# Kernel tuning notes

Hardware: AMD Instinct MI355X
Metric: run time of the kernel (lower is better)

The kernel has to match this reference:

```python
import jax, jax.numpy as jnp
import numpy as np
from jax import lax

# --- constants matching init_kwargs ---
NUM_SCALES = 3
LAMBDA_0, MU_0 = 1.0, 0.5
KAPPA_LAMBDA, KAPPA_MU = 2.0, 1.0
BASE_WEIGHT, GRADIENT_SCALING = 1.0, 5.0
CLAMP_MIN, CLAMP_MAX = 0.1, 10.0
SCALE_WEIGHTS = [1.0, 0.5, 0.25]
JAC_PENALTY_W = 0.1
BLUR_KSIZE, BLUR_SIGMA = 5, 1.1  # torchvision default sigma for ksize=5: 0.3*((5-1)*0.5-1)+0.8


def _resize1d_align_corners(x, axis, out_size):
    """Linear resize along one axis with align_corners=True (separable trilinear)."""
    n = x.shape[axis]
    if out_size == n:
        return x
    coords = jnp.arange(out_size, dtype=jnp.float32) * ((n - 1) / max(out_size - 1, 1))
    i0 = jnp.floor(coords).astype(jnp.int32)
    i1 = jnp.minimum(i0 + 1, n - 1)
    w = (coords - i0.astype(jnp.float32)).astype(x.dtype)
    shape = [1] * x.ndim
    shape[axis] = out_size
    w = w.reshape(shape)
    x0 = jnp.take(x, i0, axis=axis)
    x1 = jnp.take(x, i1, axis=axis)
    return x0 * (1 - w) + x1 * w


def trilinear_resize(x, out_sizes):
    # x: (B, C, X, Y, Z); align_corners=True trilinear is separable
    for ax, s in zip((-3, -2, -1), out_sizes):
        x = _resize1d_align_corners(x, ax % x.ndim, s)
    return x


def _blur_axis(x, axis, k):
    r = (BLUR_KSIZE - 1) // 2
    pad = [(0, 0)] * x.ndim
    pad[axis] = (r, r)
    xp = jnp.pad(x, pad, mode='reflect')
    n = x.shape[axis]
    out = jnp.zeros_like(x)
    for t in range(BLUR_KSIZE):
        out = out + k[t] * lax.slice_in_dim(xp, t, t + n, axis=axis)
    return out


def gaussian_blur3d(x):
    t = jnp.arange(BLUR_KSIZE, dtype=jnp.float32) - (BLUR_KSIZE - 1) / 2
    k = jnp.exp(-(t ** 2) / (2.0 * BLUR_SIGMA ** 2))
    k = (k / k.sum()).astype(x.dtype)
    for ax in (-3, -2, -1):
        x = _blur_axis(x, ax % x.ndim, k)
    return x


def jacobian_penalty(deform):
    # 3x3 Jacobian of the displacement at the center voxel via central differences
    B, _, X, Y, Z = deform.shape
    c = (X // 2, Y // 2, Z // 2)
    dx = 0.5 * (deform[:, :, c[0] + 1, c[1], c[2]] - deform[:, :, c[0] - 1, c[1], c[2]])
    dy = 0.5 * (deform[:, :, c[0], c[1] + 1, c[2]] - deform[:, :, c[0], c[1] - 1, c[2]])
    dz = 0.5 * (deform[:, :, c[0], c[1], c[2] + 1] - deform[:, :, c[0], c[1], c[2] - 1])
    J = jnp.stack([dx, dy, dz], axis=-1)  # (B, 3, 3)
    det = jnp.linalg.det(J)
    return jnp.mean(jax.nn.relu(-det))


def _loss_fwd(deformation_field, image):
    B, _, X, Y, Z = deformation_field.shape
    total = jnp.zeros((), dtype=deformation_field.dtype)
    for i in range(NUM_SCALES):
        scale = 2 ** i
        out_sizes = (X // scale, Y // scale, Z // scale)
        deform_s = trilinear_resize(deformation_field, out_sizes)
        image_s = trilinear_resize(image, out_sizes)
        img = image_s[:, 0]  # (B, x, y, z)
        gx, gy, gz = jnp.gradient(img, axis=(-3, -2, -1))
        image_gradient = jnp.sqrt(gx ** 2 + gy ** 2 + gz ** 2)
        ig_sm = gaussian_blur3d(image_gradient[None])  # (1, B, x, y, z)
        lam = jnp.clip(LAMBDA_0 + KAPPA_LAMBDA * ig_sm, CLAMP_MIN, CLAMP_MAX)
        mu = jnp.clip(MU_0 + KAPPA_MU * ig_sm, CLAMP_MIN, CLAMP_MAX)
        du = jnp.gradient(deform_s[:, 0], axis=(-3, -2, -1))
        dv = jnp.gradient(deform_s[:, 1], axis=(-3, -2, -1))
        dw = jnp.gradient(deform_s[:, 2], axis=(-3, -2, -1))
        E_xx, E_yy, E_zz = du[0], dv[1], dw[2]
        E_xy = 0.5 * (du[1] + dv[0])
        E_xz = 0.5 * (du[2] + dw[0])
        E_yz = 0.5 * (dv[2] + dw[1])
        trace_E = E_xx + E_yy + E_zz
        energy = (0.5 * lam * trace_E ** 2
                  + mu * (E_xx ** 2 + E_yy ** 2 + E_zz ** 2
                          + 2.0 * (E_xy ** 2 + E_xz ** 2 + E_yz ** 2)))
        weight = BASE_WEIGHT + GRADIENT_SCALING * ig_sm
        total = total + SCALE_WEIGHTS[i] * jnp.mean(weight * energy)
    total = total + JAC_PENALTY_W * jacobian_penalty(deformation_field)
    return total


def setup_inputs() -> dict:
    key = jax.random.key(0)
    k1, k2 = jax.random.split(key)
    deformation_field = jax.random.normal(k1, (2, 3, 160, 160, 160), dtype=jnp.float32)
    image = jax.random.uniform(k2, (2, 1, 160, 160, 160), dtype=jnp.float32)
    return {"deformation_field": deformation_field, "image": image}


def reference(deformation_field, image):
    return _loss_fwd(deformation_field, image)
```

## Files before the change

### kernel.cpp

```cpp
#include <hip/hip_runtime.h>

#define TPB 256

#define K0 0.0707663f
#define K1 0.2444606f
#define K2 0.3695462f

#define EB0 8000
#define EB1 1000
#define EB2 125
#define BB0 2000
#define BB1 250
#define BB2 32

typedef float f4 __attribute__((ext_vector_type(4)));

__device__ __forceinline__ f4 ld4(const float* __restrict__ p) { return *(const f4*)p; }

__device__ __forceinline__ int rref(int i, int n) {
    return i < 0 ? -i : (i >= n ? 2 * n - 2 - i : i);
}

template <int NIN, int M>
__device__ __forceinline__ void resize_one(const float* __restrict__ in,
                                           float* __restrict__ out, long idx) {
    constexpr float ratio = (float)((NIN - 1.0) / (M - 1.0));
    int z = (int)(idx % M); long r = idx / M;
    int y = (int)(r % M);   r /= M;
    int x = (int)(r % M);   int bc = (int)(r / M);

    float cx = (float)x * ratio, cy = (float)y * ratio, cz = (float)z * ratio;
    int x0 = min((int)cx, NIN - 1), y0 = min((int)cy, NIN - 1), z0 = min((int)cz, NIN - 1);
    float wx = cx - (float)x0, wy = cy - (float)y0, wz = cz - (float)z0;
    int x1 = min(x0 + 1, NIN - 1), y1 = min(y0 + 1, NIN - 1), z1 = min(z0 + 1, NIN - 1);

    const float* p = in + (long)bc * NIN * NIN * NIN;
    constexpr long sx = (long)NIN * NIN;
#define AT(xi, yi, zi) p[(long)(xi) * sx + (long)(yi) * NIN + (zi)]
    float c00 = AT(x0, y0, z0) * (1.f - wz) + AT(x0, y0, z1) * wz;
    float c01 = AT(x0, y1, z0) * (1.f - wz) + AT(x0, y1, z1) * wz;
    float c10 = AT(x1, y0, z0) * (1.f - wz) + AT(x1, y0, z1) * wz;
    float c11 = AT(x1, y1, z0) * (1.f - wz) + AT(x1, y1, z1) * wz;
#undef AT
    float c0 = c00 * (1.f - wy) + c01 * wy;
    float c1 = c10 * (1.f - wy) + c11 * wy;
    out[idx] = c0 * (1.f - wx) + c1 * wx;
}

__global__ __launch_bounds__(TPB)
void resize_all_kernel(const float* __restrict__ D, const float* __restrict__ I,
                       float* __restrict__ ds1, float* __restrict__ ds2,
                       float* __restrict__ is1, float* __restrict__ is2,
                       long A, long Bn, long C, long Dn) {
    long idx = (long)blockIdx.x * blockDim.x + threadIdx.x;
    if (idx < A) { resize_one<160, 80>(D, ds1, idx); return; }
    idx -= A;
    if (idx < Bn) { resize_one<160, 40>(D, ds2, idx); return; }
    idx -= Bn;
    if (idx < C) { resize_one<160, 80>(I, is1, idx); return; }
    idx -= C;
    if (idx < Dn) { resize_one<160, 40>(I, is2, idx); }
}

template <int N>
__device__ __forceinline__ void gradmag_one(const float* __restrict__ img,
                                            float* __restrict__ g, long idx) {
    constexpr int NZ4 = N / 4;
    constexpr long n2 = (long)N * N, n3 = n2 * N;
    int z4 = (int)(idx % NZ4); long r = idx / NZ4;
    int y = (int)(r % N); r /= N;
    int x = (int)(r % N); int b = (int)(r / N);
    int z = z4 * 4;

    const float* base = img + (long)b * n3;
    const float* rowc = base + (long)x * n2 + (long)y * N;
    f4 cur = ld4(rowc + z);
    f4 prev = (z > 0) ? ld4(rowc + z - 4) : cur;
    f4 next = (z + 4 < N) ? ld4(rowc + z + 4) : cur;

    int xm = max(x - 1, 0), xp = min(x + 1, N - 1);
    int ym = max(y - 1, 0), yp = min(y + 1, N - 1);
    float hx = (x == 0 || x == N - 1) ? 1.f : 0.5f;
    float hy = (y == 0 || y == N - 1) ? 1.f : 0.5f;
    f4 rxp = ld4(base + (long)xp * n2 + (long)y * N + z);
    f4 rxm = ld4(base + (long)xm * n2 + (long)y * N + z);
    f4 ryp = ld4(base + (long)x * n2 + (long)yp * N + z);
    f4 rym = ld4(base + (long)x * n2 + (long)ym * N + z);

    f4 outv;
#pragma unroll
    for (int j = 0; j < 4; ++j) {
        float c = cur[j];
        float zmv = (j == 0) ? prev[3] : cur[(j == 0) ? 0 : j - 1];
        float zpv = (j == 3) ? next[0] : cur[(j == 3) ? 3 : j + 1];
        int gz = z + j;
        float dz = (gz == 0) ? (zpv - c) : ((gz == N - 1) ? (c - zmv) : 0.5f * (zpv - zmv));
        float dx = hx * (rxp[j] - rxm[j]);
        float dy = hy * (ryp[j] - rym[j]);
        outv[j] = sqrtf(dx * dx + dy * dy + dz * dz);
    }
    *(f4*)(g + (long)b * n3 + (long)x * n2 + (long)y * N + z) = outv;
}

__global__ __launch_bounds__(TPB)
void gradmag_all(const float* __restrict__ I0, const float* __restrict__ is1,
                 const float* __restrict__ is2, float* __restrict__ g0,
                 float* __restrict__ g1, float* __restrict__ g2) {
    int blk = blockIdx.x;
    if (blk < EB0)            gradmag_one<160>(I0,  g0, (long)blk * TPB + threadIdx.x);
    else if (blk < EB0 + EB1) gradmag_one<80> (is1, g1, (long)(blk - EB0) * TPB + threadIdx.x);
    else                      gradmag_one<40> (is2, g2, (long)(blk - EB0 - EB1) * TPB + threadIdx.x);
}

template <int N>
__device__ __forceinline__ void blur_one(const float* __restrict__ in,
                                         float* __restrict__ out, long idx) {
    constexpr int NZ4 = N / 4, NY4 = N / 4;
    constexpr long n2 = (long)N * N, n3 = n2 * N;
    int z4 = (int)(idx % NZ4); long r = idx / NZ4;
    int y4 = (int)(r % NY4); r /= NY4;
    int x = (int)(r % N); int b = (int)(r / N);
    int y0 = y4 * 4, z = z4 * 4;

    const float K[5] = {K0, K1, K2, K1, K0};
    const float* base = in + (long)b * n3 + z;

    f4 cs[8];
#pragma unroll
    for (int jj = 0; jj < 8; ++jj) cs[jj] = (f4){0.f, 0.f, 0.f, 0.f};

#pragma unroll
    for (int i = 0; i < 5; ++i) {
        int qx = rref(x + i - 2, N);
        const float* px = base + (long)qx * n2;
#pragma unroll
        for (int jj = 0; jj < 8; ++jj) {
            int qy = rref(y0 - 2 + jj, N);
            cs[jj] += K[i] * ld4(px + (long)qy * N);
        }
    }
    float* ob = out + (long)b * n3 + (long)x * n2 + z;
#pragma unroll
    for (int k = 0; k < 4; ++k) {
        f4 o = K0 * cs[k] + K1 * cs[k + 1] + K2 * cs[k + 2] + K1 * cs[k + 3] + K0 * cs[k + 4];
        *(f4*)(ob + (long)(y0 + k) * N) = o;
    }
}

__global__ __launch_bounds__(TPB)
void blur_all(const float* __restrict__ g0, const float* __restrict__ g1,
              const float* __restrict__ g2, float* __restrict__ t0,
              float* __restrict__ t1, float* __restrict__ t2) {
    int blk = blockIdx.x;
    if (blk < BB0)            blur_one<160>(g0, t0, (long)blk * TPB + threadIdx.x);
    else if (blk < BB0 + BB1) blur_one<80> (g1, t1, (long)(blk - BB0) * TPB + threadIdx.x);
    else {
        long idx = (long)(blk - BB0 - BB1) * TPB + threadIdx.x;
        if (idx < (long)2 * 40 * 10 * 10) blur_one<40>(g2, t2, idx);
    }
}

template <int N>
__device__ __forceinline__ float energy_one(const float* __restrict__ def,
                                            const float* __restrict__ igxy, long idx) {
    constexpr int NZ4 = N / 4;
    constexpr long n2 = (long)N * N, n3 = n2 * N;
    int z4 = (int)(idx % NZ4); long r = idx / NZ4;
    int y = (int)(r % N); r /= N;
    int x = (int)(r % N); int b = (int)(r / N);
    int z = z4 * 4;

    int xm = max(x - 1, 0), xp = min(x + 1, N - 1);
    int ym = max(y - 1, 0), yp = min(y + 1, N - 1);
    float hx = (x == 0 || x == N - 1) ? 1.f : 0.5f;
    float hy = (y == 0 || y == N - 1) ? 1.f : 0.5f;

    const float* base = def + (long)b * 3 * n3;
    long sp = (long)x * n2 + (long)y * N + z;

    f4 CC[3], CP[3], CN[3], RXP[3], RXM[3], RYP[3], RYM[3];
#pragma unroll
    for (int c = 0; c < 3; ++c) {
        const float* rc = base + (long)c * n3 + sp;
        CC[c] = ld4(rc);
        CP[c] = (z > 0) ? ld4(rc - 4) : CC[c];
        CN[c] = (z + 4 < N) ? ld4(rc + 4) : CC[c];
        RXP[c] = ld4(base + (long)c * n3 + (long)xp * n2 + (long)y * N + z);
        RXM[c] = ld4(base + (long)c * n3 + (long)xm * n2 + (long)y * N + z);
        RYP[c] = ld4(base + (long)c * n3 + (long)x * n2 + (long)yp * N + z);
        RYM[c] = ld4(base + (long)c * n3 + (long)x * n2 + (long)ym * N + z);
    }

    const float* growc = igxy + (long)b * n3 + (long)x * n2 + (long)y * N;
    f4 gcur = ld4(growc + z);
    f4 gprev, gnext;
    if (z >= 4) gprev = ld4(growc + z - 4);
    else { gprev[0] = growc[4]; gprev[1] = growc[3]; gprev[2] = growc[2]; gprev[3] = growc[1]; }
    if (z + 8 <= N) gnext = ld4(growc + z + 4);
    else { gnext[0] = growc[N - 2]; gnext[1] = growc[N - 3]; gnext[2] = growc[N - 4]; gnext[3] = growc[N - 5]; }
    float gw[12];
#pragma unroll
    for (int i = 0; i < 4; ++i) { gw[i] = gprev[i]; gw[4 + i] = gcur[i]; gw[8 + i] = gnext[i]; }

    float lsum = 0.f;
#pragma unroll
    for (int j = 0; j < 4; ++j) {
        int gz = z + j;
        float dX[3], dY[3], dZ[3];
#pragma unroll
        for (int c = 0; c < 3; ++c) {
            float cc = CC[c][j];
            float zmv = (j == 0) ? CP[c][3] : CC[c][(j == 0) ? 0 : j - 1];
            float zpv = (j == 3) ? CN[c][0] : CC[c][(j == 3) ? 3 : j + 1];
            dZ[c] = (gz == 0) ? (zpv - cc)
                              : ((gz == N - 1) ? (cc - zmv) : 0.5f * (zpv - zmv));
            dX[c] = hx * (RXP[c][j] - RXM[c][j]);
            dY[c] = hy * (RYP[c][j] - RYM[c][j]);
        }
        float igv = K0 * gw[2 + j] + K1 * gw[3 + j] + K2 * gw[4 + j]
                  + K1 * gw[5 + j] + K0 * gw[6 + j];
        float lam = fminf(fmaxf(1.0f + 2.0f * igv, 0.1f), 10.0f);
        float mu  = fminf(fmaxf(0.5f + 1.0f * igv, 0.1f), 10.0f);
        float wt  = 1.0f + 5.0f * igv;

        float Exx = dX[0], Eyy = dY[1], Ezz = dZ[2];
        float Exy = 0.5f * (dY[0] + dX[1]);
        float Exz = 0.5f * (dZ[0] + dX[2]);
        float Eyz = 0.5f * (dZ[1] + dY[2]);
        float tr = Exx + Eyy + Ezz;
        float e = 0.5f * lam * tr * tr +
                  mu * (Exx * Exx + Eyy * Eyy + Ezz * Ezz +
                        2.0f * (Exy * Exy + Exz * Exz + Eyz * Eyz));
        lsum += wt * e;
    }
    return lsum;
}

__global__ __launch_bounds__(TPB)
void energy_all(const float* __restrict__ D, const float* __restrict__ ds1,
                const float* __restrict__ ds2, const float* __restrict__ t0,
                const float* __restrict__ t1, const float* __restrict__ t2,
                float* __restrict__ partial) {
    int blk = blockIdx.x;
    float lsum;
    if (blk < EB0)            lsum = energy_one<160>(D,   t0, (long)blk * TPB + threadIdx.x);
    else if (blk < EB0 + EB1) lsum = energy_one<80> (ds1, t1, (long)(blk - EB0) * TPB + threadIdx.x);
    else                      lsum = energy_one<40> (ds2, t2, (long)(blk - EB0 - EB1) * TPB + threadIdx.x);

    __shared__ float sm[TPB];
    sm[threadIdx.x] = lsum;
    __syncthreads();
    for (int s = TPB / 2; s > 0; s >>= 1) {
        if (threadIdx.x < s) sm[threadIdx.x] += sm[threadIdx.x + s];
        __syncthreads();
    }
    if (threadIdx.x == 0) partial[blk] = sm[0];
}

__global__ __launch_bounds__(TPB)
void finalize_kernel(const float* __restrict__ partial,
                     const float* __restrict__ def, float* __restrict__ out) {
    __shared__ float sm[TPB];
    const float wts[3] = {1.0f, 0.5f, 0.25f};
    const float invcnt[3] = {1.0f / (2.0f * 160 * 160 * 160),
                             1.0f / (2.0f * 80 * 80 * 80),
                             1.0f / (2.0f * 40 * 40 * 40)};
    const int offs[3] = {0, EB0, EB0 + EB1};
    const int cnts[3] = {EB0, EB1, EB2};
    float acc = 0.f;
    for (int s = 0; s < 3; ++s) {
        float local = 0.f;
        for (int i = threadIdx.x; i < cnts[s]; i += TPB) local += partial[offs[s] + i];
        acc += wts[s] * invcnt[s] * local;
    }
    sm[threadIdx.x] = acc;
    __syncthreads();
    for (int s = TPB / 2; s > 0; s >>= 1) {
        if (threadIdx.x < s) sm[threadIdx.x] += sm[threadIdx.x + s];
        __syncthreads();
    }
    if (threadIdx.x == 0) {
        float jac = 0.f;
        const int n = 160;
        long n3 = (long)n * n * n;
        long ctr = ((long)80 * n + 80) * n + 80;
        for (int b = 0; b < 2; ++b) {
            const float* p = def + (long)b * 3 * n3;
            float J[3][3];
            for (int c = 0; c < 3; ++c) {
                const float* q = p + (long)c * n3 + ctr;
                J[c][0] = 0.5f * (q[(long)n * n] - q[-(long)n * n]);
                J[c][1] = 0.5f * (q[n] - q[-n]);
                J[c][2] = 0.5f * (q[1] - q[-1]);
            }
            float det = J[0][0] * (J[1][1] * J[2][2] - J[1][2] * J[2][1])
                      - J[0][1] * (J[1][0] * J[2][2] - J[1][2] * J[2][0])
                      + J[0][2] * (J[1][0] * J[2][1] - J[1][1] * J[2][0]);
            jac += fmaxf(-det, 0.f);
        }
        jac *= 0.5f;
        out[0] = sm[0] + 0.1f * jac;
    }
}

extern "C" void kernel_launch(void* const* d_in, const int* in_sizes, int n_in,
                              void* d_out, int out_size, void* d_ws, size_t ws_size,
                              hipStream_t stream) {
    const float* D = (const float*)d_in[0];
    const float* I = (const float*)d_in[1];
    float* out = (float*)d_out;
    float* ws = (float*)d_ws;

    const int B = 2;
    const long S0 = (long)B * 160 * 160 * 160;
    const long S1 = (long)B * 80 * 80 * 80;
    const long S2 = (long)B * 40 * 40 * 40;

    float* partials = ws;
    float* ds1 = partials + 9216;
    float* is1 = ds1 + 3 * S1;
    float* g1  = is1 + S1;
    float* t1  = g1 + S1;
    float* ds2 = t1 + S1;
    float* is2 = ds2 + 3 * S2;
    float* g2  = is2 + S2;
    float* t2  = g2 + S2;
    float* g0  = t2 + S2;
    float* t0  = g0 + S0;

    {
        long A = 3 * S1, Bn = 3 * S2, C = S1, Dn = S2;
        long tot = A + Bn + C + Dn;
        resize_all_kernel<<<(int)((tot + TPB - 1) / TPB), TPB, 0, stream>>>(
            D, I, ds1, ds2, is1, is2, A, Bn, C, Dn);
    }
    gradmag_all<<<EB0 + EB1 + EB2, TPB, 0, stream>>>(I, is1, is2, g0, g1, g2);
    blur_all<<<BB0 + BB1 + BB2, TPB, 0, stream>>>(g0, g1, g2, t0, t1, t2);
    energy_all<<<EB0 + EB1 + EB2, TPB, 0, stream>>>(D, ds1, ds2, t0, t1, t2, partials);
    finalize_kernel<<<1, TPB, 0, stream>>>(partials, D, out);
}
```

Baseline: 163.7 us.

## Process four y-rows per thread in gradmag and energy, two outputs per resize thread

Gradient-magnitude and energy kernels now have each thread walk four consecutive y rows, carrying the y-1/y/y+1 rows in registers so neighbouring-row loads are reused instead of reloaded. The resize kernel assigns two output elements per thread using fixed compile-time split constants. Grid sizes and partial-buffer layout are adjusted to match. This cuts redundant global loads and thread count, at the cost of more registers per thread and fewer waves to hide latency.

```diff
diff --git a/kernel.cpp b/kernel.cpp
--- a/kernel.cpp
+++ b/kernel.cpp
@@ -6,12 +6,14 @@
 #define K1 0.2444606f
 #define K2 0.3695462f
 
-#define EB0 8000
-#define EB1 1000
-#define EB2 125
+#define GB0 2000
+#define GB1 250
+#define GB2 32
 #define BB0 2000
 #define BB1 250
 #define BB2 32
+#define RHALF 2304000L
+#define RBLK 9000
 
 typedef float f4 __attribute__((ext_vector_type(4)));
 
@@ -47,59 +49,77 @@
     out[idx] = c0 * (1.f - wx) + c1 * wx;
 }
 
+__device__ __forceinline__ void resize_dispatch(const float* __restrict__ D,
+                                                const float* __restrict__ I,
+                                                float* __restrict__ ds1, float* __restrict__ ds2,
+                                                float* __restrict__ is1, float* __restrict__ is2,
+                                                long idx) {
+    if (idx < 3072000L) { resize_one<160, 80>(D, ds1, idx); return; }
+    idx -= 3072000L;
+    if (idx < 384000L) { resize_one<160, 40>(D, ds2, idx); return; }
+    idx -= 384000L;
+    if (idx < 1024000L) { resize_one<160, 80>(I, is1, idx); return; }
+    idx -= 1024000L;
+    resize_one<160, 40>(I, is2, idx);
+}
+
 __global__ __launch_bounds__(TPB)
 void resize_all_kernel(const float* __restrict__ D, const float* __restrict__ I,
                        float* __restrict__ ds1, float* __restrict__ ds2,
-                       float* __restrict__ is1, float* __restrict__ is2,
-                       long A, long Bn, long C, long Dn) {
-    long idx = (long)blockIdx.x * blockDim.x + threadIdx.x;
-    if (idx < A) { resize_one<160, 80>(D, ds1, idx); return; }
-    idx -= A;
-    if (idx < Bn) { resize_one<160, 40>(D, ds2, idx); return; }
-    idx -= Bn;
-    if (idx < C) { resize_one<160, 80>(I, is1, idx); return; }
-    idx -= C;
-    if (idx < Dn) { resize_one<160, 40>(I, is2, idx); }
+                       float* __restrict__ is1, float* __restrict__ is2) {
+    long idx = (long)blockIdx.x * TPB + threadIdx.x;
+    resize_dispatch(D, I, ds1, ds2, is1, is2, idx);
+    resize_dispatch(D, I, ds1, ds2, is1, is2, idx + RHALF);
 }
 
 template <int N>
-__device__ __forceinline__ void gradmag_one(const float* __restrict__ img,
-                                            float* __restrict__ g, long idx) {
-    constexpr int NZ4 = N / 4;
+__device__ __forceinline__ void gradmag_y4(const float* __restrict__ img,
+                                           float* __restrict__ g, long idx) {
+    constexpr int NZ4 = N / 4, NY4 = N / 4;
     constexpr long n2 = (long)N * N, n3 = n2 * N;
     int z4 = (int)(idx % NZ4); long r = idx / NZ4;
-    int y = (int)(r % N); r /= N;
+    int y4 = (int)(r % NY4); r /= NY4;
     int x = (int)(r % N); int b = (int)(r / N);
-    int z = z4 * 4;
+    int y0 = y4 * 4, z = z4 * 4;
+
+    int xm = max(x - 1, 0), xp = min(x + 1, N - 1);
+    float hx = (x == 0 || x == N - 1) ? 1.f : 0.5f;
 
     const float* base = img + (long)b * n3;
-    const float* rowc = base + (long)x * n2 + (long)y * N;
-    f4 cur = ld4(rowc + z);
-    f4 prev = (z > 0) ? ld4(rowc + z - 4) : cur;
-    f4 next = (z + 4 < N) ? ld4(rowc + z + 4) : cur;
-
-    int xm = max(x - 1, 0), xp = min(x + 1, N - 1);
-    int ym = max(y - 1, 0), yp = min(y + 1, N - 1);
-    float hx = (x == 0 || x == N - 1) ? 1.f : 0.5f;
-    float hy = (y == 0 || y == N - 1) ? 1.f : 0.5f;
-    f4 rxp = ld4(base + (long)xp * n2 + (long)y * N + z);
-    f4 rxm = ld4(base + (long)xm * n2 + (long)y * N + z);
-    f4 ryp = ld4(base + (long)x * n2 + (long)yp * N + z);
-    f4 rym = ld4(base + (long)x * n2 + (long)ym * N + z);
-
-    f4 outv;
-#pragma unroll
-    for (int j = 0; j < 4; ++j) {
-        float c = cur[j];
-        float zmv = (j == 0) ? prev[3] : cur[(j == 0) ? 0 : j - 1];
-        float zpv = (j == 3) ? next[0] : cur[(j == 3) ? 3 : j + 1];
-        int gz = z + j;
-        float dz = (gz == 0) ? (zpv - c) : ((gz == N - 1) ? (c - zmv) : 0.5f * (zpv - zmv));
-        float dx = hx * (rxp[j] - rxm[j]);
-        float dy = hy * (ryp[j] - rym[j]);
-        outv[j] = sqrtf(dx * dx + dy * dy + dz * dz);
-    }
-    *(f4*)(g + (long)b * n3 + (long)x * n2 + (long)y * N + z) = outv;
+    const float* colx = base + (long)x * n2;
+    float* gb = g + (long)b * n3 + (long)x * n2 + z;
+
+    f4 Im = ld4(colx + (long)max(y0 - 1, 0) * N + z);
+    f4 Ic = ld4(colx + (long)y0 * N + z);
+
+#pragma unroll
+    for (int jy = 0; jy < 4; ++jy) {
+        int y = y0 + jy;
+        int yp = min(y + 1, N - 1);
+        float hy = (y == 0 || y == N - 1) ? 1.f : 0.5f;
+        f4 Ip = ld4(colx + (long)yp * N + z);
+        const float* rowy = colx + (long)y * N;
+        f4 prev = (z > 0) ? ld4(rowy + z - 4) : Ic;
+        f4 next = (z + 4 < N) ? ld4(rowy + z + 4) : Ic;
+        f4 rxp = ld4(base + (long)xp * n2 + (long)y * N + z);
+        f4 rxm = ld4(base + (long)xm * n2 + (long)y * N + z);
+
+        f4 outv;
+#pragma unroll
+        for (int j = 0; j < 4; ++j) {
+            float c = Ic[j];
+            float zmv = (j == 0) ? prev[3] : Ic[(j == 0) ? 0 : j - 1];
+            float zpv = (j == 3) ? next[0] : Ic[(j == 3) ? 3 : j + 1];
+            int gz = z + j;
+            float dz = (gz == 0) ? (zpv - c) : ((gz == N - 1) ? (c - zmv) : 0.5f * (zpv - zmv));
+            float dx = hx * (rxp[j] - rxm[j]);
+            float dy = hy * (Ip[j] - Im[j]);
+            outv[j] = sqrtf(dx * dx + dy * dy + dz * dz);
+        }
+        *(f4*)(gb + (long)y * N) = outv;
+
+        Im = Ic; Ic = Ip;
+    }
 }
 
 __global__ __launch_bounds__(TPB)
@@ -107,9 +127,12 @@
                  const float* __restrict__ is2, float* __restrict__ g0,
                  float* __restrict__ g1, float* __restrict__ g2) {
     int blk = blockIdx.x;
-    if (blk < EB0)            gradmag_one<160>(I0,  g0, (long)blk * TPB + threadIdx.x);
-    else if (blk < EB0 + EB1) gradmag_one<80> (is1, g1, (long)(blk - EB0) * TPB + threadIdx.x);
-    else                      gradmag_one<40> (is2, g2, (long)(blk - EB0 - EB1) * TPB + threadIdx.x);
+    if (blk < GB0)            gradmag_y4<160>(I0,  g0, (long)blk * TPB + threadIdx.x);
+    else if (blk < GB0 + GB1) gradmag_y4<80> (is1, g1, (long)(blk - GB0) * TPB + threadIdx.x);
+    else {
+        long idx = (long)(blk - GB0 - GB1) * TPB + threadIdx.x;
+        if (idx < 8000) gradmag_y4<40>(is2, g2, idx);
+    }
 }
 
 template <int N>
@@ -156,82 +179,98 @@
     else if (blk < BB0 + BB1) blur_one<80> (g1, t1, (long)(blk - BB0) * TPB + threadIdx.x);
     else {
         long idx = (long)(blk - BB0 - BB1) * TPB + threadIdx.x;
-        if (idx < (long)2 * 40 * 10 * 10) blur_one<40>(g2, t2, idx);
+        if (idx < 8000) blur_one<40>(g2, t2, idx);
     }
 }
 
 template <int N>
-__device__ __forceinline__ float energy_one(const float* __restrict__ def,
-                                            const float* __restrict__ igxy, long idx) {
-    constexpr int NZ4 = N / 4;
+__device__ __forceinline__ float energy_y4(const float* __restrict__ def,
+                                           const float* __restrict__ igxy, long idx) {
+    constexpr int NZ4 = N / 4, NY4 = N / 4;
     constexpr long n2 = (long)N * N, n3 = n2 * N;
     int z4 = (int)(idx % NZ4); long r = idx / NZ4;
-    int y = (int)(r % N); r /= N;
+    int y4 = (int)(r % NY4); r /= NY4;
     int x = (int)(r % N); int b = (int)(r / N);
-    int z = z4 * 4;
+    int y0 = y4 * 4, z = z4 * 4;
 
     int xm = max(x - 1, 0), xp = min(x + 1, N - 1);
-    int ym = max(y - 1, 0), yp = min(y + 1, N - 1);
     float hx = (x == 0 || x == N - 1) ? 1.f : 0.5f;
-    float hy = (y == 0 || y == N - 1) ? 1.f : 0.5f;
 
     const float* base = def + (long)b * 3 * n3;
-    long sp = (long)x * n2 + (long)y * N + z;
-
-    f4 CC[3], CP[3], CN[3], RXP[3], RXM[3], RYP[3], RYM[3];
+    const float* igcol = igxy + (long)b * n3 + (long)x * n2;
+
+    f4 CCm[3], CCc[3];
+    int ymi = max(y0 - 1, 0);
 #pragma unroll
     for (int c = 0; c < 3; ++c) {
-        const float* rc = base + (long)c * n3 + sp;
-        CC[c] = ld4(rc);
-        CP[c] = (z > 0) ? ld4(rc - 4) : CC[c];
-        CN[c] = (z + 4 < N) ? ld4(rc + 4) : CC[c];
-        RXP[c] = ld4(base + (long)c * n3 + (long)xp * n2 + (long)y * N + z);
-        RXM[c] = ld4(base + (long)c * n3 + (long)xm * n2 + (long)y * N + z);
-        RYP[c] = ld4(base + (long)c * n3 + (long)x * n2 + (long)yp * N + z);
-        RYM[c] = ld4(base + (long)c * n3 + (long)x * n2 + (long)ym * N + z);
-    }
-
-    const float* growc = igxy + (long)b * n3 + (long)x * n2 + (long)y * N;
-    f4 gcur = ld4(growc + z);
-    f4 gprev, gnext;
-    if (z >= 4) gprev = ld4(growc + z - 4);
-    else { gprev[0] = growc[4]; gprev[1] = growc[3]; gprev[2] = growc[2]; gprev[3] = growc[1]; }
-    if (z + 8 <= N) gnext = ld4(growc + z + 4);
-    else { gnext[0] = growc[N - 2]; gnext[1] = growc[N - 3]; gnext[2] = growc[N - 4]; gnext[3] = growc[N - 5]; }
-    float gw[12];
-#pragma unroll
-    for (int i = 0; i < 4; ++i) { gw[i] = gprev[i]; gw[4 + i] = gcur[i]; gw[8 + i] = gnext[i]; }
+        const float* rc = base + (long)c * n3 + (long)x * n2;
+        CCm[c] = ld4(rc + (long)ymi * N + z);
+        CCc[c] = ld4(rc + (long)y0 * N + z);
+    }
 
     float lsum = 0.f;
 #pragma unroll
-    for (int j = 0; j < 4; ++j) {
-        int gz = z + j;
-        float dX[3], dY[3], dZ[3];
+    for (int jy = 0; jy < 4; ++jy) {
+        int y = y0 + jy;
+        int yp = min(y + 1, N - 1);
+        float hy = (y == 0 || y == N - 1) ? 1.f : 0.5f;
+
+        f4 CCp[3], CPc[3], CNc[3], RXP[3], RXM[3];
 #pragma unroll
         for (int c = 0; c < 3; ++c) {
-            float cc = CC[c][j];
-            float zmv = (j == 0) ? CP[c][3] : CC[c][(j == 0) ? 0 : j - 1];
-            float zpv = (j == 3) ? CN[c][0] : CC[c][(j == 3) ? 3 : j + 1];
-            dZ[c] = (gz == 0) ? (zpv - cc)
-                              : ((gz == N - 1) ? (cc - zmv) : 0.5f * (zpv - zmv));
-            dX[c] = hx * (RXP[c][j] - RXM[c][j]);
-            dY[c] = hy * (RYP[c][j] - RYM[c][j]);
-        }
-        float igv = K0 * gw[2 + j] + K1 * gw[3 + j] + K2 * gw[4 + j]
-                  + K1 * gw[5 + j] + K0 * gw[6 + j];
-        float lam = fminf(fmaxf(1.0f + 2.0f * igv, 0.1f), 10.0f);
-        float mu  = fminf(fmaxf(0.5f + 1.0f * igv, 0.1f), 10.0f);
-        float wt  = 1.0f + 5.0f * igv;
-
-        float Exx = dX[0], Eyy = dY[1], Ezz = dZ[2];
-        float Exy = 0.5f * (dY[0] + dX[1]);
-        float Exz = 0.5f * (dZ[0] + dX[2]);
-        float Eyz = 0.5f * (dZ[1] + dY[2]);
-        float tr = Exx + Eyy + Ezz;
-        float e = 0.5f * lam * tr * tr +
-                  mu * (Exx * Exx + Eyy * Eyy + Ezz * Ezz +
-                        2.0f * (Exy * Exy + Exz * Exz + Eyz * Eyz));
-        lsum += wt * e;
+            const float* rc = base + (long)c * n3;
+            const float* rcy = rc + (long)x * n2 + (long)y * N;
+            CCp[c] = ld4(rc + (long)x * n2 + (long)yp * N + z);
+            CPc[c] = (z > 0) ? ld4(rcy + z - 4) : CCc[c];
+            CNc[c] = (z + 4 < N) ? ld4(rcy + z + 4) : CCc[c];
+            RXP[c] = ld4(rc + (long)xp * n2 + (long)y * N + z);
+            RXM[c] = ld4(rc + (long)xm * n2 + (long)y * N + z);
+        }
+
+        const float* growc = igcol + (long)y * N;
+        f4 gc = ld4(growc + z);
+        f4 gp, gn;
+        if (z >= 4) gp = ld4(growc + z - 4);
+        else { gp[0] = growc[4]; gp[1] = growc[3]; gp[2] = growc[2]; gp[3] = growc[1]; }
+        if (z + 8 <= N) gn = ld4(growc + z + 4);
+        else { gn[0] = growc[N - 2]; gn[1] = growc[N - 3]; gn[2] = growc[N - 4]; gn[3] = growc[N - 5]; }
+        float gw[12];
+#pragma unroll
+        for (int i = 0; i < 4; ++i) { gw[i] = gp[i]; gw[4 + i] = gc[i]; gw[8 + i] = gn[i]; }
+
+#pragma unroll
+        for (int j = 0; j < 4; ++j) {
+            int gz = z + j;
+            float dX[3], dY[3], dZ[3];
+#pragma unroll
+            for (int c = 0; c < 3; ++c) {
+                float cc = CCc[c][j];
+                float zmv = (j == 0) ? CPc[c][3] : CCc[c][(j == 0) ? 0 : j - 1];
+                float zpv = (j == 3) ? CNc[c][0] : CCc[c][(j == 3) ? 3 : j + 1];
+                dZ[c] = (gz == 0) ? (zpv - cc)
+                                  : ((gz == N - 1) ? (cc - zmv) : 0.5f * (zpv - zmv));
+                dX[c] = hx * (RXP[c][j] - RXM[c][j]);
+                dY[c] = hy * (CCp[c][j] - CCm[c][j]);
+            }
+            float igv = K0 * gw[2 + j] + K1 * gw[3 + j] + K2 * gw[4 + j]
+                      + K1 * gw[5 + j] + K0 * gw[6 + j];
+            float lam = fminf(fmaxf(1.0f + 2.0f * igv, 0.1f), 10.0f);
+            float mu  = fminf(fmaxf(0.5f + 1.0f * igv, 0.1f), 10.0f);
+            float wt  = 1.0f + 5.0f * igv;
+
+            float Exx = dX[0], Eyy = dY[1], Ezz = dZ[2];
+            float Exy = 0.5f * (dY[0] + dX[1]);
+            float Exz = 0.5f * (dZ[0] + dX[2]);
+            float Eyz = 0.5f * (dZ[1] + dY[2]);
+            float tr = Exx + Eyy + Ezz;
+            float e = 0.5f * lam * tr * tr +
+                      mu * (Exx * Exx + Eyy * Eyy + Ezz * Ezz +
+                            2.0f * (Exy * Exy + Exz * Exz + Eyz * Eyz));
+            lsum += wt * e;
+        }
+
+#pragma unroll
+        for (int c = 0; c < 3; ++c) { CCm[c] = CCc[c]; CCc[c] = CCp[c]; }
     }
     return lsum;
 }
@@ -242,10 +281,13 @@
                 const float* __restrict__ t1, const float* __restrict__ t2,
                 float* __restrict__ partial) {
     int blk = blockIdx.x;
-    float lsum;
-    if (blk < EB0)            lsum = energy_one<160>(D,   t0, (long)blk * TPB + threadIdx.x);
-    else if (blk < EB0 + EB1) lsum = energy_one<80> (ds1, t1, (long)(blk - EB0) * TPB + threadIdx.x);
-    else                      lsum = energy_one<40> (ds2, t2, (long)(blk - EB0 - EB1) * TPB + threadIdx.x);
+    float lsum = 0.f;
+    if (blk < GB0)            lsum = energy_y4<160>(D,   t0, (long)blk * TPB + threadIdx.x);
+    else if (blk < GB0 + GB1) lsum = energy_y4<80> (ds1, t1, (long)(blk - GB0) * TPB + threadIdx.x);
+    else {
+        long idx = (long)(blk - GB0 - GB1) * TPB + threadIdx.x;
+        if (idx < 8000) lsum = energy_y4<40>(ds2, t2, idx);
+    }
 
     __shared__ float sm[TPB];
     sm[threadIdx.x] = lsum;
@@ -265,8 +307,8 @@
     const float invcnt[3] = {1.0f / (2.0f * 160 * 160 * 160),
                              1.0f / (2.0f * 80 * 80 * 80),
                              1.0f / (2.0f * 40 * 40 * 40)};
-    const int offs[3] = {0, EB0, EB0 + EB1};
-    const int cnts[3] = {EB0, EB1, EB2};
+    const int offs[3] = {0, GB0, GB0 + GB1};
+    const int cnts[3] = {GB0, GB1, GB2};
     float acc = 0.f;
     for (int s = 0; s < 3; ++s) {
         float local = 0.f;
@@ -317,7 +359,7 @@
     const long S2 = (long)B * 40 * 40 * 40;
 
     float* partials = ws;
-    float* ds1 = partials + 9216;
+    float* ds1 = partials + 4096;
     float* is1 = ds1 + 3 * S1;
     float* g1  = is1 + S1;
     float* t1  = g1 + S1;
@@ -328,14 +370,9 @@
     float* g0  = t2 + S2;
     float* t0  = g0 + S0;
 
-    {
-        long A = 3 * S1, Bn = 3 * S2, C = S1, Dn = S2;
-        long tot = A + Bn + C + Dn;
-        resize_all_kernel<<<(int)((tot + TPB - 1) / TPB), TPB, 0, stream>>>(
-            D, I, ds1, ds2, is1, is2, A, Bn, C, Dn);
-    }
-    gradmag_all<<<EB0 + EB1 + EB2, TPB, 0, stream>>>(I, is1, is2, g0, g1, g2);
+    resize_all_kernel<<<RBLK, TPB, 0, stream>>>(D, I, ds1, ds2, is1, is2);
+    gradmag_all<<<GB0 + GB1 + GB2, TPB, 0, stream>>>(I, is1, is2, g0, g1, g2);
     blur_all<<<BB0 + BB1 + BB2, TPB, 0, stream>>>(g0, g1, g2, t0, t1, t2);
-    energy_all<<<EB0 + EB1 + EB2, TPB, 0, stream>>>(D, ds1, ds2, t0, t1, t2, partials);
+    energy_all<<<GB0 + GB1 + GB2, TPB, 0, stream>>>(D, ds1, ds2, t0, t1, t2, partials);
     finalize_kernel<<<1, TPB, 0, stream>>>(partials, D, out);
 }
```

New measurement: 182.5 us. 1.11x slower.
